# Kernel optimization log

Measured on AMD Instinct MI355X. Metric: run time of the kernel, lower is better.

Reference implementation:

```python
import jax, jax.numpy as jnp
import numpy as np

NEG = -1.0e9

def setup_inputs() -> dict:
    key = jax.random.key(0)
    ks = jax.random.split(key, 4)
    B, S, D, DK = 4, 2048, 1024, 128
    inputs = jax.random.normal(ks[0], (B, S, D), dtype=jnp.float32)
    scale = 1.0 / np.sqrt(D)
    Wq = jax.random.normal(ks[1], (D, DK), dtype=jnp.float32) * scale
    Wk = jax.random.normal(ks[2], (D, DK), dtype=jnp.float32) * scale
    Wv = jax.random.normal(ks[3], (D, DK), dtype=jnp.float32) * scale
    bq = jnp.zeros((DK,), dtype=jnp.float32)
    bk = jnp.zeros((DK,), dtype=jnp.float32)
    bv = jnp.zeros((DK,), dtype=jnp.float32)
    return {"inputs": inputs, "Wq": Wq, "bq": bq, "Wk": Wk, "bk": bk, "Wv": Wv, "bv": bv}

def reference(inputs, Wq, bq, Wk, bk, Wv, bv):
    # Q/K/V projections: Dense(d_k) on last dim
    Q = jnp.einsum('bsd,dk->bsk', inputs, Wq) + bq
    K = jnp.einsum('bsd,dk->bsk', inputs, Wk) + bk
    V = jnp.einsum('bsd,dk->bsk', inputs, Wv) + bv
    d_k = Q.shape[-1]
    S = inputs.shape[1]
    # FAITHFUL to original bug: mask = lower-triangular ones, added *-1e9
    # (masks the lower triangle including the diagonal, NOT the upper).
    mask = jnp.tril(jnp.ones((S, S), dtype=inputs.dtype))
    scores = jnp.einsum('bqk,bsk->bqs', Q, K) / jnp.sqrt(jnp.asarray(d_k, inputs.dtype))
    masked_scores = scores + mask * NEG  # [B, S, S]
    attn = jax.nn.softmax(masked_scores, axis=-1)
    out = jnp.einsum('bqs,bsk->bqk', attn, V)  # [B, S, d_k]
    return out
```

## Files before the change

### kernel.cpp

```cpp
#include <hip/hip_runtime.h>
#include <hip/hip_bf16.h>

typedef __attribute__((ext_vector_type(8))) short bf16x8;
typedef __attribute__((ext_vector_type(4))) float f32x4;

#define QSCALE 0.088388347648318447f

__device__ __forceinline__ unsigned short f2bf(float f) {
  __hip_bfloat16 h = __float2bfloat16(f);
  unsigned short u;
  __builtin_memcpy(&u, &h, 2);
  return u;
}
__device__ __forceinline__ float bf2f(unsigned short u) {
  unsigned int x = ((unsigned int)u) << 16;
  float f; __builtin_memcpy(&f, &x, 4);
  return f;
}

__device__ __forceinline__ void gload_lds16(void* lds, const void* g) {
  __builtin_amdgcn_global_load_lds(
      (const __attribute__((address_space(1))) unsigned int*)g,
      (__attribute__((address_space(3))) unsigned int*)lds, 16, 0, 0);
}

__global__ __launch_bounds__(256) void cvt(const float* __restrict__ x,
                                           unsigned short* __restrict__ xb,
                                           const float* __restrict__ Wq,
                                           const float* __restrict__ Wk,
                                           const float* __restrict__ Wv,
                                           unsigned short* __restrict__ Wt) {
  const int bid = blockIdx.x;
  if (bid < 4096) {
    int i = (bid * 256 + threadIdx.x) * 8;
    float4 v0 = *reinterpret_cast<const float4*>(x + i);
    float4 v1 = *reinterpret_cast<const float4*>(x + i + 4);
    ushort4 o0, o1;
    o0.x = f2bf(v0.x); o0.y = f2bf(v0.y); o0.z = f2bf(v0.z); o0.w = f2bf(v0.w);
    o1.x = f2bf(v1.x); o1.y = f2bf(v1.y); o1.z = f2bf(v1.z); o1.w = f2bf(v1.w);
    *reinterpret_cast<ushort4*>(xb + i) = o0;
    *reinterpret_cast<ushort4*>(xb + i + 4) = o1;
  } else {
    int idx = (bid - 4096) * 256 + threadIdx.x;
    int n = idx >> 10, d = idx & 1023;
    const float* W = (n < 128) ? Wq : (n < 256 ? Wk : Wv);
    float v = W[d * 128 + (n & 127)];
    if (n < 128) v *= QSCALE;
    Wt[idx] = f2bf(v);
  }
}

__global__ __launch_bounds__(256) void proj_gemm(
    const unsigned short* __restrict__ Xb, const unsigned short* __restrict__ Wt,
    const float* __restrict__ bq, const float* __restrict__ bk, const float* __restrict__ bv,
    unsigned short* __restrict__ Qb, unsigned short* __restrict__ Kb,
    unsigned short* __restrict__ Vt) {
  __shared__ unsigned short sA[64 * 64];
  __shared__ unsigned short sB[64 * 64];
  const int nt = blockIdx.x % 6;
  const int mt = blockIdx.x / 6;
  const int m0 = mt * 64;
  const int n0 = nt * 64;
  const int tid = threadIdx.x;
  const int lane = tid & 63;
  const int w = tid >> 6;
  const int r = lane & 15, g = lane >> 4;
  const int wm = (w >> 1) * 32, wn = (w & 1) * 32;

  f32x4 acc[2][2];
  #pragma unroll
  for (int mi = 0; mi < 2; ++mi)
    #pragma unroll
    for (int ni = 0; ni < 2; ++ni)
      acc[mi][ni] = (f32x4){0.f, 0.f, 0.f, 0.f};

  const char* Ab = (const char*)Xb;
  const char* Bb = (const char*)Wt;
  char* sAb = (char*)sA;
  char* sBb = (char*)sB;

  for (int k0 = 0; k0 < 1024; k0 += 64) {
    #pragma unroll
    for (int j = 0; j < 2; ++j) {
      int f = j * 4096 + tid * 16;
      int row = f >> 7;
      int colb = f & 127;
      gload_lds16(sAb + f, Ab + ((size_t)(m0 + row) * 1024 + k0) * 2 + colb);
      gload_lds16(sBb + f, Bb + ((size_t)(n0 + row) * 1024 + k0) * 2 + colb);
    }
    __syncthreads();
    #pragma unroll
    for (int kk = 0; kk < 2; ++kk) {
      bf16x8 af[2], bfr[2];
      #pragma unroll
      for (int mi = 0; mi < 2; ++mi)
        af[mi] = *reinterpret_cast<const bf16x8*>(sA + (wm + mi * 16 + r) * 64 + kk * 32 + g * 8);
      #pragma unroll
      for (int ni = 0; ni < 2; ++ni)
        bfr[ni] = *reinterpret_cast<const bf16x8*>(sB + (wn + ni * 16 + r) * 64 + kk * 32 + g * 8);
      #pragma unroll
      for (int mi = 0; mi < 2; ++mi)
        #pragma unroll
        for (int ni = 0; ni < 2; ++ni)
          acc[mi][ni] = __builtin_amdgcn_mfma_f32_16x16x32_bf16(af[mi], bfr[ni], acc[mi][ni], 0, 0, 0);
    }
    __syncthreads();
  }

  const float* bias = (nt < 2) ? bq : (nt < 4 ? bk : bv);
  const float bsc = (nt < 2) ? QSCALE : 1.0f;
  #pragma unroll
  for (int mi = 0; mi < 2; ++mi) {
    #pragma unroll
    for (int ni = 0; ni < 2; ++ni) {
      const int colg = n0 + wn + ni * 16 + r;
      const int colm = colg & 127;
      const float bias_v = bias[colm] * bsc;
      #pragma unroll
      for (int e = 0; e < 4; ++e) {
        const int row = m0 + wm + mi * 16 + g * 4 + e;
        const unsigned short hh = f2bf(acc[mi][ni][e] + bias_v);
        if (nt < 2) Qb[(size_t)row * 128 + colm] = hh;
        else if (nt < 4) Kb[(size_t)row * 128 + colm] = hh;
        else {
          const int bb = row >> 11, s = row & 2047;
          Vt[((size_t)bb * 128 + colm) * 2048 + s] = hh;
        }
      }
    }
  }
}

__global__ __launch_bounds__(256, 4) void attn(
    const unsigned short* __restrict__ Qb, const unsigned short* __restrict__ Kb,
    const unsigned short* __restrict__ Vt,
    unsigned short* __restrict__ po, float* __restrict__ pl) {
  __shared__ char sK[2][8192];
  __shared__ char sV[2][8192];
  __shared__ unsigned short pbuf_s[4][512];
  const int tid = threadIdx.x;
  const int lane = tid & 63;
  const int w = tid >> 6;
  const int r = lane & 15, g = lane >> 4;
  const int sig = blockIdx.x & 7;
  const int b = (blockIdx.x >> 3) & 3;
  const int p = (blockIdx.x >> 5) & 7;
  const int h2 = blockIdx.x >> 8;

  const char* Kg = (const char*)(Kb + (size_t)b * 2048 * 128);
  const char* Vg = (const char*)(Vt + (size_t)b * 128 * 2048);
  unsigned short* pbuf = pbuf_s[w];

  const int kr0 = tid >> 4;
  const int kr1 = 16 + (tid >> 4);
  const int kc0 = ((tid & 15) * 16) ^ ((kr0 & 7) * 16);
  const int kc1 = ((tid & 15) * 16) ^ ((kr1 & 7) * 16);
  const int vr0 = tid >> 2;
  const int vr1 = 64 + (tid >> 2);
  const int vc0 = ((tid & 3) * 16) ^ ((vr0 & 3) * 16);
  const int vc1 = ((tid & 3) * 16) ^ ((vr1 & 3) * 16);

  for (int phase = 0; phase < 2; ++phase) {
    const int t = phase ? (15 - p) : p;
    const int sb = t * 128 + h2 * 64;
    const int ntiles = (2048 - sb) >> 5;
    const int q0w = t * 128 + h2 * 64 + w * 16;

    const unsigned short* Q = Qb + (size_t)(b * 2048 + q0w) * 128;
    bf16x8 qf[4];
    #pragma unroll
    for (int kk = 0; kk < 4; ++kk)
      qf[kk] = *reinterpret_cast<const bf16x8*>(Q + r * 128 + kk * 32 + g * 8);

    f32x4 o[8];
    #pragma unroll
    for (int ni = 0; ni < 8; ++ni) o[ni] = (f32x4){0.f, 0.f, 0.f, 0.f};
    float l[4];
    #pragma unroll
    for (int e = 0; e < 4; ++e) l[e] = 0.f;

    const int nT = (ntiles > sig) ? ((ntiles - sig + 7) >> 3) : 0;

    if (nT > 0) {
      const int s0 = sb + (sig << 5);
      gload_lds16(&sK[0][tid * 16], Kg + (size_t)(s0 + kr0) * 256 + kc0);
      gload_lds16(&sK[0][4096 + tid * 16], Kg + (size_t)(s0 + kr1) * 256 + kc1);
      gload_lds16(&sV[0][tid * 16], Vg + (size_t)vr0 * 4096 + (size_t)s0 * 2 + vc0);
      gload_lds16(&sV[0][4096 + tid * 16], Vg + (size_t)vr1 * 4096 + (size_t)s0 * 2 + vc1);
    }
    for (int it = 0; it < nT; ++it) {
      const int cur = it & 1;
      const int s0 = sb + ((sig + (it << 3)) << 5);
      asm volatile("s_waitcnt vmcnt(0) lgkmcnt(0)" ::: "memory");
      __builtin_amdgcn_sched_barrier(0);
      asm volatile("s_barrier" ::: "memory");
      if (it + 1 < nT) {
        const int s1 = s0 + 256;
        gload_lds16(&sK[cur ^ 1][tid * 16], Kg + (size_t)(s1 + kr0) * 256 + kc0);
        gload_lds16(&sK[cur ^ 1][4096 + tid * 16], Kg + (size_t)(s1 + kr1) * 256 + kc1);
        gload_lds16(&sV[cur ^ 1][tid * 16], Vg + (size_t)vr0 * 4096 + (size_t)s1 * 2 + vc0);
        gload_lds16(&sV[cur ^ 1][4096 + tid * 16], Vg + (size_t)vr1 * 4096 + (size_t)s1 * 2 + vc1);
      }

      f32x4 st[2];
      #pragma unroll
      for (int sj = 0; sj < 2; ++sj) {
        f32x4 a = (f32x4){0.f, 0.f, 0.f, 0.f};
        #pragma unroll
        for (int kk = 0; kk < 4; ++kk) {
          const bf16x8 kf = *reinterpret_cast<const bf16x8*>(
              &sK[cur][(sj * 16 + r) * 256 + (((kk * 64 + g * 16) ^ ((r & 7) * 16)))]);
          a = __builtin_amdgcn_mfma_f32_16x16x32_bf16(qf[kk], kf, a, 0, 0, 0);
        }
        st[sj] = a;
      }
      #pragma unroll
      for (int sj = 0; sj < 2; ++sj) {
        const int s = s0 + sj * 16 + r;
        #pragma unroll
        for (int e = 0; e < 4; ++e) {
          const int q = q0w + g * 4 + e;
          st[sj][e] = (s <= q) ? 0.f : __expf(st[sj][e]);
        }
      }
      #pragma unroll
      for (int e = 0; e < 4; ++e) l[e] += st[0][e] + st[1][e];

      #pragma unroll
      for (int sj = 0; sj < 2; ++sj)
        #pragma unroll
        for (int e = 0; e < 4; ++e)
          pbuf[(g * 4 + e) * 32 + sj * 16 + r] = f2bf(st[sj][e]);
      asm volatile("s_waitcnt lgkmcnt(0)" ::: "memory");
      __builtin_amdgcn_sched_barrier(0);
      const bf16x8 pa = *reinterpret_cast<const bf16x8*>(&pbuf[r * 32 + g * 8]);

      #pragma unroll
      for (int ni = 0; ni < 8; ++ni) {
        const bf16x8 vf = *reinterpret_cast<const bf16x8*>(
            &sV[cur][(ni * 16 + r) * 64 + ((g * 16) ^ ((r & 3) * 16))]);
        o[ni] = __builtin_amdgcn_mfma_f32_16x16x32_bf16(pa, vf, o[ni], 0, 0, 0);
      }
    }

    #pragma unroll
    for (int off = 1; off < 16; off <<= 1)
      #pragma unroll
      for (int e = 0; e < 4; ++e)
        l[e] += __shfl_xor(l[e], off, 64);

    const size_t pb = ((size_t)((b * 16 + t) * 8 + sig)) * 16384;
    const int rbase = h2 * 64 + w * 16;
    #pragma unroll
    for (int ni = 0; ni < 8; ++ni)
      #pragma unroll
      for (int e = 0; e < 4; ++e)
        po[pb + (size_t)(rbase + g * 4 + e) * 128 + ni * 16 + r] = f2bf(o[ni][e]);
    if (r == 0) {
      #pragma unroll
      for (int e = 0; e < 4; ++e)
        pl[((size_t)((b * 16 + t) * 8 + sig)) * 128 + rbase + g * 4 + e] = l[e];
    }
    __syncthreads();
  }
}

__global__ __launch_bounds__(256) void combine(const unsigned short* __restrict__ po,
                                               const float* __restrict__ pl,
                                               const unsigned short* __restrict__ Vt,
                                               float* __restrict__ out) {
  const int bid = blockIdx.x;
  if (bid < 4096) {
    const int idx = bid * 256 + threadIdx.x;
    const int d = idx & 127;
    const int gq = idx >> 7;
    const int b = gq >> 11, q = gq & 2047;
    if (q == 2047) return;
    const int qt = q >> 7, row = q & 127;
    const size_t base = (size_t)(b * 16 + qt) * 8;
    float o = 0.f, l = 0.f;
    #pragma unroll
    for (int s = 0; s < 8; ++s) {
      o += bf2f(po[(base + s) * 16384 + row * 128 + d]);
      l += pl[(base + s) * 128 + row];
    }
    out[idx] = (l > 0.f) ? o / l : 0.f;
  } else {
    const int seg = bid - 4096;
    const int b = seg >> 5;
    const int w = threadIdx.x >> 6;
    const int lane = threadIdx.x & 63;
    const int dk = (seg & 31) * 4 + w;
    const unsigned short* row = Vt + (size_t)(b * 128 + dk) * 2048;
    float s = 0.f;
    for (int i = lane; i < 2048; i += 64) s += bf2f(row[i]);
    #pragma unroll
    for (int off = 32; off > 0; off >>= 1) s += __shfl_down(s, off, 64);
    if (lane == 0) out[(size_t)(b * 2048 + 2047) * 128 + dk] = s * (1.0f / 2048.0f);
  }
}

extern "C" void kernel_launch(void* const* d_in, const int* in_sizes, int n_in,
                              void* d_out, int out_size, void* d_ws, size_t ws_size,
                              hipStream_t stream) {
  const float* x  = (const float*)d_in[0];
  const float* Wq = (const float*)d_in[1];
  const float* bq = (const float*)d_in[2];
  const float* Wk = (const float*)d_in[3];
  const float* bk = (const float*)d_in[4];
  const float* Wv = (const float*)d_in[5];
  const float* bv = (const float*)d_in[6];
  float* out = (float*)d_out;
  char* ws = (char*)d_ws;
  unsigned short* Xb = (unsigned short*)(ws);
  unsigned short* Wt = (unsigned short*)(ws + (size_t)(16u << 20));
  unsigned short* Qb = (unsigned short*)(ws + (size_t)(17u << 20));
  unsigned short* Kb = (unsigned short*)(ws + (size_t)(19u << 20));
  unsigned short* Vt = (unsigned short*)(ws + (size_t)(21u << 20));
  unsigned short* po = (unsigned short*)(ws + (size_t)(24u << 20));
  float* pl = (float*)(ws + (size_t)(48u << 20));

  hipLaunchKernelGGL(cvt, dim3(5632), dim3(256), 0, stream, x, Xb, Wq, Wk, Wv, Wt);
  hipLaunchKernelGGL(proj_gemm, dim3(768), dim3(256), 0, stream,
                     Xb, Wt, bq, bk, bv, Qb, Kb, Vt);
  hipLaunchKernelGGL(attn, dim3(512), dim3(256), 0, stream, Qb, Kb, Vt, po, pl);
  hipLaunchKernelGGL(combine, dim3(4224), dim3(256), 0, stream, po, pl, Vt, out);
}
```

Measured before the change: 64.08 us.

## Fuse fp32-to-bf16 input conversion into projection GEMM A-tile load

Removes the separate pass that converts the 32MB fp32 input to a bf16 workspace copy. The projection GEMM now loads fp32 X tiles directly, converts them in registers and stores bf16 into shared memory, while weights still come from a small conversion kernel. Block indexing changes so that the six N-tiles sharing an M-tile are spread apart and the m-tiles of one n-tile are consecutive. The trade-off is that each X tile is now read in fp32 by six blocks instead of in bf16, and the async global-to-LDS load for A becomes a synchronous register path.

```diff
diff --git a/kernel.cpp b/kernel.cpp
--- a/kernel.cpp
+++ b/kernel.cpp
@@ -24,41 +24,27 @@
       (__attribute__((address_space(3))) unsigned int*)lds, 16, 0, 0);
 }
 
-__global__ __launch_bounds__(256) void cvt(const float* __restrict__ x,
-                                           unsigned short* __restrict__ xb,
-                                           const float* __restrict__ Wq,
-                                           const float* __restrict__ Wk,
-                                           const float* __restrict__ Wv,
-                                           unsigned short* __restrict__ Wt) {
-  const int bid = blockIdx.x;
-  if (bid < 4096) {
-    int i = (bid * 256 + threadIdx.x) * 8;
-    float4 v0 = *reinterpret_cast<const float4*>(x + i);
-    float4 v1 = *reinterpret_cast<const float4*>(x + i + 4);
-    ushort4 o0, o1;
-    o0.x = f2bf(v0.x); o0.y = f2bf(v0.y); o0.z = f2bf(v0.z); o0.w = f2bf(v0.w);
-    o1.x = f2bf(v1.x); o1.y = f2bf(v1.y); o1.z = f2bf(v1.z); o1.w = f2bf(v1.w);
-    *reinterpret_cast<ushort4*>(xb + i) = o0;
-    *reinterpret_cast<ushort4*>(xb + i + 4) = o1;
-  } else {
-    int idx = (bid - 4096) * 256 + threadIdx.x;
-    int n = idx >> 10, d = idx & 1023;
-    const float* W = (n < 128) ? Wq : (n < 256 ? Wk : Wv);
-    float v = W[d * 128 + (n & 127)];
-    if (n < 128) v *= QSCALE;
-    Wt[idx] = f2bf(v);
-  }
+__global__ __launch_bounds__(256) void cvt_w(const float* __restrict__ Wq,
+                                             const float* __restrict__ Wk,
+                                             const float* __restrict__ Wv,
+                                             unsigned short* __restrict__ Wt) {
+  int idx = blockIdx.x * 256 + threadIdx.x;
+  int n = idx >> 10, d = idx & 1023;
+  const float* W = (n < 128) ? Wq : (n < 256 ? Wk : Wv);
+  float v = W[d * 128 + (n & 127)];
+  if (n < 128) v *= QSCALE;
+  Wt[idx] = f2bf(v);
 }
 
 __global__ __launch_bounds__(256) void proj_gemm(
-    const unsigned short* __restrict__ Xb, const unsigned short* __restrict__ Wt,
+    const float* __restrict__ X, const unsigned short* __restrict__ Wt,
     const float* __restrict__ bq, const float* __restrict__ bk, const float* __restrict__ bv,
     unsigned short* __restrict__ Qb, unsigned short* __restrict__ Kb,
     unsigned short* __restrict__ Vt) {
   __shared__ unsigned short sA[64 * 64];
   __shared__ unsigned short sB[64 * 64];
-  const int nt = blockIdx.x % 6;
-  const int mt = blockIdx.x / 6;
+  const int mt = blockIdx.x & 127;
+  const int nt = blockIdx.x >> 7;
   const int m0 = mt * 64;
   const int n0 = nt * 64;
   const int tid = threadIdx.x;
@@ -74,19 +60,25 @@
     for (int ni = 0; ni < 2; ++ni)
       acc[mi][ni] = (f32x4){0.f, 0.f, 0.f, 0.f};
 
-  const char* Ab = (const char*)Xb;
   const char* Bb = (const char*)Wt;
-  char* sAb = (char*)sA;
   char* sBb = (char*)sB;
 
   for (int k0 = 0; k0 < 1024; k0 += 64) {
     #pragma unroll
     for (int j = 0; j < 2; ++j) {
       int f = j * 4096 + tid * 16;
-      int row = f >> 7;
-      int colb = f & 127;
-      gload_lds16(sAb + f, Ab + ((size_t)(m0 + row) * 1024 + k0) * 2 + colb);
+      int row = f >> 7, colb = f & 127;
       gload_lds16(sBb + f, Bb + ((size_t)(n0 + row) * 1024 + k0) * 2 + colb);
+    }
+    #pragma unroll
+    for (int it2 = 0; it2 < 4; ++it2) {
+      const int f = it2 * 1024 + tid * 4;
+      const int row = f >> 6, col = f & 63;
+      const float4 v = *reinterpret_cast<const float4*>(
+          X + (size_t)(m0 + row) * 1024 + k0 + col);
+      ushort4 o4;
+      o4.x = f2bf(v.x); o4.y = f2bf(v.y); o4.z = f2bf(v.z); o4.w = f2bf(v.w);
+      *reinterpret_cast<ushort4*>(&sA[row * 64 + col]) = o4;
     }
     __syncthreads();
     #pragma unroll
@@ -312,7 +304,6 @@
   const float* bv = (const float*)d_in[6];
   float* out = (float*)d_out;
   char* ws = (char*)d_ws;
-  unsigned short* Xb = (unsigned short*)(ws);
   unsigned short* Wt = (unsigned short*)(ws + (size_t)(16u << 20));
   unsigned short* Qb = (unsigned short*)(ws + (size_t)(17u << 20));
   unsigned short* Kb = (unsigned short*)(ws + (size_t)(19u << 20));
@@ -320,9 +311,9 @@
   unsigned short* po = (unsigned short*)(ws + (size_t)(24u << 20));
   float* pl = (float*)(ws + (size_t)(48u << 20));
 
-  hipLaunchKernelGGL(cvt, dim3(5632), dim3(256), 0, stream, x, Xb, Wq, Wk, Wv, Wt);
+  hipLaunchKernelGGL(cvt_w, dim3(1536), dim3(256), 0, stream, Wq, Wk, Wv, Wt);
   hipLaunchKernelGGL(proj_gemm, dim3(768), dim3(256), 0, stream,
-                     Xb, Wt, bq, bk, bv, Qb, Kb, Vt);
+                     x, Wt, bq, bk, bv, Qb, Kb, Vt);
   hipLaunchKernelGGL(attn, dim3(512), dim3(256), 0, stream, Qb, Kb, Vt, po, pl);
   hipLaunchKernelGGL(combine, dim3(4224), dim3(256), 0, stream, po, pl, Vt, out);
 }
```

Measured after the change: 72.37 us. +12.9%, slower.
